# Kernel optimization log

Hardware: AMD Instinct MI355X
Metric: run time of the kernel (lower is better)

Reference implementation:

```python
import jax, jax.numpy as jnp
import numpy as np

B, T, V, H = 512, 200, 99, 256


def setup_inputs() -> dict:
    key = jax.random.key(0)
    ks = jax.random.split(key, 32)
    u01 = lambda k, shp, s: jax.random.uniform(k, shp, jnp.float32, -s, s)
    sV = 1.0 / np.sqrt(V); sH = 1.0 / np.sqrt(H); s2V = 1.0 / np.sqrt(2 * V)
    inp = {
        'x': jax.random.normal(ks[0], (B, T, V), jnp.float32),
        'x_hat': jax.random.normal(ks[1], (B, T, V), jnp.float32),
        'u': jax.random.uniform(ks[2], (B, T, V), jnp.float32),
        'm': (jax.random.uniform(ks[3], (B, T, V)) < 0.8).astype(jnp.float32),  # observation mask
        'd': jax.random.uniform(ks[4], (B, T, V), jnp.float32) * 5.0,  # time deltas >= 0
        'y': jax.random.uniform(ks[5], (B, 1), jnp.float32),
        'W_td': u01(ks[6], (H, V), sV), 'b_td': u01(ks[7], (H,), sV),
        'W_hist': u01(ks[8], (V, H), sH), 'b_hist': u01(ks[9], (V,), sH),
        'W_v': u01(ks[10], (V, V), sV), 'b_v': u01(ks[11], (V,), sV),
        'W_r': u01(ks[12], (V, V), sV), 'b_r': u01(ks[13], (V,), sV),
        'W_u': u01(ks[14], (V, V), sV), 'b_u': u01(ks[15], (V,), sV),
        'conv_w': u01(ks[16], (2,), 1.0 / np.sqrt(2.0)), 'conv_b': u01(ks[17], (1,), 1.0 / np.sqrt(2.0)),
        'W_ih': u01(ks[18], (3 * H, 2 * V), s2V), 'b_ih': u01(ks[19], (3 * H,), s2V),
        'W_hh': u01(ks[20], (3 * H, H), sH), 'b_hh': u01(ks[21], (3 * H,), sH),
        'W_fc': u01(ks[22], (1, H), sH), 'b_fc': u01(ks[23], (1,), sH),
    }
    return inp


def _rin_forward(x, x_hat, u, m, d,
                 W_td, b_td, W_hist, b_hist, W_v, b_v, W_r, b_r, W_u, b_u,
                 conv_w, conv_b, W_ih, b_ih, W_hh, b_hh, W_fc, b_fc):
    mfr = 1.0 - jnp.eye(V, dtype=x.dtype)
    Wv_m = (W_v * mfr).T
    Wr_m = (W_r * mfr).T
    h0 = jnp.zeros((x.shape[0], H), x.dtype)

    def step(carry, inp_t):
        h, loss = carry
        x_t, xh_t, u_t, m_t, d_t = inp_t
        gamma_h = jnp.exp(-jax.nn.relu(d_t @ W_td.T + b_td))  # [B,H]
        h = h * gamma_h
        x_h = h @ W_hist.T + b_hist                            # [B,V]
        x_r_t = m_t * x_t + (1.0 - m_t) * x_h
        xbar = m_t * x_t + (1.0 - m_t) * xh_t
        unc = jnp.exp(-jax.nn.relu(u_t @ W_u.T + b_u))         # unc_flag == 1
        xu = (xbar @ Wv_m + b_v) * unc
        xr = x_r_t @ Wr_m + b_r
        x_comb = conv_w[0] * xu + conv_w[1] * xr + conv_b[0]   # 1x1 conv over channel dim 2
        loss = loss + jnp.sum(jnp.abs(x_t - x_comb) * m_t) / (jnp.sum(m_t) + 1e-5)
        x_imp_t = m_t * x_t + (1.0 - m_t) * x_comb
        gru_in = jnp.concatenate([x_imp_t, m_t], axis=1)       # [B,2V]
        gi = gru_in @ W_ih.T + b_ih                            # [B,3H]
        gh = h @ W_hh.T + b_hh
        r = jax.nn.sigmoid(gi[:, :H] + gh[:, :H])
        z = jax.nn.sigmoid(gi[:, H:2 * H] + gh[:, H:2 * H])
        n = jnp.tanh(gi[:, 2 * H:] + r * gh[:, 2 * H:])
        h = (1.0 - z) * n + z * h
        return (h, loss), (x_imp_t, xu, xr)

    seq = (jnp.swapaxes(x, 0, 1), jnp.swapaxes(x_hat, 0, 1), jnp.swapaxes(u, 0, 1),
           jnp.swapaxes(m, 0, 1), jnp.swapaxes(d, 0, 1))  # [T,B,V] each
    (h, x_loss), (x_imp, xus, xrs) = jax.lax.scan(step, (h0, jnp.float32(0.0)), seq)
    x_imp = jnp.swapaxes(x_imp, 0, 1)  # [B,T,V]
    xus = jnp.swapaxes(xus, 0, 1)
    xrs = jnp.swapaxes(xrs, 0, 1)
    y_out = h @ W_fc.T + b_fc          # task == 'C'
    y_score = jax.nn.sigmoid(y_out)
    return x_imp, y_out, y_score, x_loss, xus, xrs


def reference(x, x_hat, u, m, d, y,
              W_td, b_td, W_hist, b_hist, W_v, b_v, W_r, b_r, W_u, b_u,
              conv_w, conv_b, W_ih, b_ih, W_hh, b_hh, W_fc, b_fc):
    return _rin_forward(x, x_hat, u, m, d,
                        W_td, b_td, W_hist, b_hist, W_v, b_v, W_r, b_r, W_u, b_u,
                        conv_w, conv_b, W_ih, b_ih, W_hh, b_hh, W_fc, b_fc)
```

## Files before the change

### kernel.cpp

```cpp
#include <hip/hip_runtime.h>

typedef unsigned short u16;
typedef unsigned int   u32;
typedef unsigned char  u8;
typedef unsigned long long u64;
typedef long i64;
typedef __attribute__((ext_vector_type(8))) short s16x8;
typedef __attribute__((ext_vector_type(4))) float f32x4;
typedef __attribute__((ext_vector_type(2))) float f32x2;
typedef __attribute__((ext_vector_type(4), aligned(4))) float f32x4u;

#define DEV static __device__ __forceinline__

constexpr int B_ = 512, T_ = 200, V_ = 99, H_ = 256;
constexpr int TV_ = T_ * V_;
constexpr u32 BH_ = B_ * H_;

constexpr long long XIMP_O = 0;
constexpr long long YOUT_O = 10137600;
constexpr long long YSC_O  = 10138112;
constexpr long long LOSS_O = 10138624;
constexpr long long XUS_O  = 10138625;
constexpr long long XRS_O  = 20276225;

constexpr long long WS_MSUM   = 0;
constexpr long long WS_GAMMA  = 1024;
constexpr long long WS_XRPRE  = 52429824;
constexpr long long WS_X16    = 72705024;
constexpr long long WS_XUS16  = 93185024;
constexpr long long WS_M8     = 113460224;
constexpr long long WS_GIM8   = 124109824;
constexpr long long WS_WTD    = 202753024;
constexpr long long WS_WU     = WS_WTD + 65536;
constexpr long long WS_WV     = WS_WU + 28672;
constexpr long long WS_WRB    = WS_WV + 28672;
constexpr long long WS_WIHM_B = WS_WRB + 28672;
constexpr long long WS_F8     = WS_WIHM_B + 196608;
constexpr long long WS_WIHX8  = WS_F8;
constexpr long long WS_WHH8   = WS_F8 + 98304;
constexpr long long WS_WHIST8 = WS_F8 + 294912;
constexpr long long WS_WR8    = WS_F8 + 323584;
constexpr long long WS_LOSSP  = WS_F8 + 337920;

DEV u16 cvt_bf16(float f) {
  union { float f; u32 u; } v; v.f = f;
  u32 u = v.u;
  return (u16)((u + 0x7fffu + ((u >> 16) & 1u)) >> 16);
}
DEV float cvt_f32(u16 h) {
  union { u32 u; float f; } v; v.u = ((u32)h) << 16;
  return v.f;
}
DEV u32 enc_e4m3(float f) {
  union { float f; u32 u; } v; v.f = f;
  u32 sign = (v.u >> 24) & 0x80u;
  v.u &= 0x7fffffffu;
  float a = fminf(v.f, 448.f);
  if (a < 0.015625f) {
    int mq = (int)rintf(a * 512.f);
    return sign | (u32)mq;
  }
  union { float f; u32 u; } w; w.f = a;
  u32 lsb = (w.u >> 20) & 1u;
  u32 r = w.u + 0x7FFFFu + lsb;
  u32 E = ((r >> 23) & 0xffu) - 120u;
  u32 M = (r >> 20) & 7u;
  if (E >= 16u) { E = 15u; M = 6u; }
  return sign | (E << 3) | M;
}
DEV u32 cvtfp8(float a) {
  u32 r;
  asm("v_cvt_pk_fp8_f32 %0, %1, %2" : "=v"(r) : "v"(a), "v"(a));
  return r;
}
DEV u32 cvtfp8x2(float a, float b) {
  u32 r;
  asm("v_cvt_pk_fp8_f32 %0, %1, %2" : "=v"(r) : "v"(a), "v"(b));
  return r & 0xffffu;
}
DEV u32 pkbf(float a, float b) {
  u32 r;
  asm("v_cvt_pk_bf16_f32 %0, %1, %2" : "=v"(r) : "v"(a), "v"(b));
  return r;
}
#if __has_builtin(__builtin_amdgcn_cvt_pk_f32_fp8)
DEV f32x4 dec8x4(u32 w) {
  f32x2 lo = __builtin_amdgcn_cvt_pk_f32_fp8((int)w, false);
  f32x2 hi = __builtin_amdgcn_cvt_pk_f32_fp8((int)w, true);
  return (f32x4){lo[0], lo[1], hi[0], hi[1]};
}
#else
DEV float dec8(u32 b) {
  u32 e = (b >> 3) & 0xfu, mm = b & 7u, s = b >> 7;
  union { u32 u; float f; } v;
  v.u = (s << 31) | ((e + 120u) << 23) | (mm << 20);
  return e ? v.f : 0.f;
}
DEV f32x4 dec8x4(u32 w) {
  return (f32x4){dec8(w & 0xff), dec8((w >> 8) & 0xff), dec8((w >> 16) & 0xff), dec8(w >> 24)};
}
#endif
DEV s16x8 mk8(f32x4 lo, f32x4 hi) {
  union { u32 q[4]; s16x8 v; } u;
  u.q[0] = pkbf(lo[0], lo[1]); u.q[1] = pkbf(lo[2], lo[3]);
  u.q[2] = pkbf(hi[0], hi[1]); u.q[3] = pkbf(hi[2], hi[3]);
  return u.v;
}
DEV f32x4 l4(const float* p) { return (f32x4)(*(const f32x4u*)p); }
DEV f32x4 mfma16(s16x8 a, s16x8 b, f32x4 c) {
  return __builtin_amdgcn_mfma_f32_16x16x32_bf16(a, b, c, 0, 0, 0);
}
DEV f32x4 mfma8(i64 a, i64 b, f32x4 c) {
  return __builtin_amdgcn_mfma_f32_16x16x32_fp8_fp8(a, b, c, 0, 0, 0);
}
DEV s16x8 ldB(const u16* w, int frag, int lane) {
  return *reinterpret_cast<const s16x8*>(w + ((long long)frag * 64 + lane) * 8);
}
DEV float sigm(float v) { return 1.f / (1.f + __expf(-v)); }
DEV float tanhx(float v) {
  float e = __expf(-2.f * fabsf(v));
  float t = (1.f - e) / (1.f + e);
  return v < 0.f ? -t : t;
}

__global__ __launch_bounds__(256) void k0_pack(
    const float* __restrict__ W_td, const float* __restrict__ W_u, const float* __restrict__ W_v,
    const float* __restrict__ W_r, const float* __restrict__ W_ih,
    float* __restrict__ msum, u16* __restrict__ wsu) {
  if (blockIdx.x == 85) {
    if (threadIdx.x < T_) msum[threadIdx.x] = 0.f;
    return;
  }
  int frag = blockIdx.x * 4 + (threadIdx.x >> 6);
  int lane = threadIdx.x & 63;
  const float* src; long long off; int koff, kmax, nmax, stride, diag = 0, f;
  if (frag < 64)       { f = frag;       src = W_td; off = WS_WTD;    stride = 99;  koff = 0;  kmax = 99; nmax = 256; }
  else if (frag < 92)  { f = frag - 64;  src = W_u;  off = WS_WU;     stride = 99;  koff = 0;  kmax = 99; nmax = 99;  }
  else if (frag < 120) { f = frag - 92;  src = W_v;  off = WS_WV;     stride = 99;  koff = 0;  kmax = 99; nmax = 99;  diag = 1; }
  else if (frag < 148) { f = frag - 120; src = W_r;  off = WS_WRB;    stride = 99;  koff = 0;  kmax = 99; nmax = 99;  diag = 1; }
  else if (frag < 340) { f = frag - 148; src = W_ih; off = WS_WIHM_B; stride = 198; koff = 99; kmax = 99; nmax = 768; }
  else return;
  int nt = f / 4, kc = f % 4;
  int n = nt * 16 + (lane & 15);
  u16* dst = wsu + off / 2 + ((long long)f * 64 + lane) * 8;
#pragma unroll
  for (int j = 0; j < 8; j++) {
    int k = kc * 32 + ((lane >> 4) << 3) + j;
    float v = 0.f;
    if (k < kmax && n < nmax && !(diag && k == n)) v = src[(long long)n * stride + koff + k];
    dst[j] = cvt_bf16(v);
  }
}

__global__ __launch_bounds__(256) void k0b_pack8(
    const float* __restrict__ W_ih, const float* __restrict__ W_hh,
    const float* __restrict__ W_hist, const float* __restrict__ W_r, u8* __restrict__ ws8) {
  int frag = blockIdx.x * 4 + (threadIdx.x >> 6);
  int lane = threadIdx.x & 63;
  const float* src; long long off; int KC, kmax, nmax, stride, diag = 0, f;
  if (frag < 192)      { f = frag;       src = W_ih;   off = WS_WIHX8;  KC = 4; stride = 198; kmax = 99;  nmax = 768; }
  else if (frag < 576) { f = frag - 192; src = W_hh;   off = WS_WHH8;   KC = 8; stride = 256; kmax = 256; nmax = 768; }
  else if (frag < 632) { f = frag - 576; src = W_hist; off = WS_WHIST8; KC = 8; stride = 256; kmax = 256; nmax = 99;  }
  else if (frag < 660) { f = frag - 632; src = W_r;    off = WS_WR8;    KC = 4; stride = 99;  kmax = 99;  nmax = 99;  diag = 1; }
  else return;
  int nt = f / KC, kc = f % KC;
  int n = nt * 16 + (lane & 15);
  u64 r = 0;
#pragma unroll
  for (int j = 0; j < 8; j++) {
    int k = kc * 32 + ((lane >> 4) << 3) + j;
    float v = 0.f;
    if (k < kmax && n < nmax && !(diag && k == n)) v = src[(long long)n * stride + k] * 16.f;
    r |= (u64)enc_e4m3(v) << (8 * j);
  }
  *reinterpret_cast<u64*>(ws8 + off + ((long long)f * 64 + lane) * 8) = r;
}

__global__ __launch_bounds__(256) void k2_pre(
    const float* __restrict__ x, const float* __restrict__ xh, const float* __restrict__ uu,
    const float* __restrict__ m, const float* __restrict__ dd,
    const float* __restrict__ b_td, const float* __restrict__ b_u, const float* __restrict__ b_v,
    const float* __restrict__ b_r, const float* __restrict__ b_ih,
    float* __restrict__ msum, float* __restrict__ out, u16* __restrict__ wsu) {
  const int tid = threadIdx.x, w = tid >> 6, lane = tid & 63;
  const int bc = blockIdx.x & 31, tg = blockIdx.x >> 5;
  const int t = tg * 4 + w;
  const int b0 = bc * 16;
  const int cl = lane & 15, rq = (lane >> 4) << 2, kr8 = (lane >> 4) << 3;
  const long long gb = (long long)(b0 + cl) * TV_ + (long long)t * V_;
  u8* ws8 = reinterpret_cast<u8*>(wsu);
  const u16* wtd   = wsu + WS_WTD / 2;
  const u16* wu    = wsu + WS_WU / 2;
  const u16* wv    = wsu + WS_WV / 2;
  const u16* wrb   = wsu + WS_WRB / 2;
  const u16* wihmb = wsu + WS_WIHM_B / 2;
  u16* gam = wsu + WS_GAMMA / 2;
  u16* xrp = wsu + WS_XRPRE / 2;
  u16* x16p = wsu + WS_X16 / 2;
  u16* xu16p = wsu + WS_XUS16 / 2;
  u8* m8p = ws8 + WS_M8;
  u8* gim8p = ws8 + WS_GIM8;
  const f32x4 z4 = {0.f, 0.f, 0.f, 0.f};

  {
    s16x8 fd[4];
#pragma unroll
    for (int kc = 0; kc < 3; kc++) {
      int k0 = kc * 32 + kr8;
      fd[kc] = mk8(l4(dd + gb + k0), l4(dd + gb + k0 + 4));
    }
    {
      f32x4 a = z4;
      if (kr8 == 0) { a[0] = dd[gb + 96]; a[1] = dd[gb + 97]; a[2] = dd[gb + 98]; }
      fd[3] = mk8(a, z4);
    }
    for (int nt = 0; nt < 16; nt++) {
      int col = nt * 16 + cl;
      float bt = b_td[col];
      f32x4 a = {bt, bt, bt, bt};
#pragma unroll
      for (int kc = 0; kc < 4; kc++) a = mfma16(fd[kc], ldB(wtd, nt * 4 + kc, lane), a);
#pragma unroll
      for (int j = 0; j < 4; j++) {
        int b = b0 + rq + j;
        gam[((long long)t * B_ + b) * H_ + col] = cvt_bf16(__expf(-fmaxf(a[j], 0.f)));
      }
    }
  }

  s16x8 fu[4], fxb[4], fmx[4], fm[4];
  float mpart = 0.f;
  const long long rowoff = (long long)t * B_ + (b0 + cl);
  u16* x16row = x16p + rowoff * 100;
  u8* m8row = m8p + rowoff * 104;
#pragma unroll
  for (int kc = 0; kc < 3; kc++) {
    int k0 = kc * 32 + kr8;
    f32x4 u0 = l4(uu + gb + k0), u1 = l4(uu + gb + k0 + 4);
    f32x4 m0 = l4(m + gb + k0),  m1 = l4(m + gb + k0 + 4);
    f32x4 x0 = l4(x + gb + k0),  x1 = l4(x + gb + k0 + 4);
    f32x4 h0 = l4(xh + gb + k0), h1 = l4(xh + gb + k0 + 4);
    fu[kc]  = mk8(u0, u1);
    fm[kc]  = mk8(m0, m1);
    fmx[kc] = mk8(m0 * x0, m1 * x1);
    fxb[kc] = mk8(h0 + m0 * (x0 - h0), h1 + m1 * (x1 - h1));
    mpart += m0[0] + m0[1] + m0[2] + m0[3] + m1[0] + m1[1] + m1[2] + m1[3];
    u64 xw0 = (u64)pkbf(x0[0], x0[1]) | ((u64)pkbf(x0[2], x0[3]) << 32);
    u64 xw1 = (u64)pkbf(x1[0], x1[1]) | ((u64)pkbf(x1[2], x1[3]) << 32);
    *reinterpret_cast<u64*>(x16row + k0) = xw0;
    *reinterpret_cast<u64*>(x16row + k0 + 4) = xw1;
    u64 mb = 0;
#pragma unroll
    for (int e = 0; e < 4; e++) {
      mb |= (m0[e] > 0.5f ? 0x50ull : 0ull) << (8 * e);
      mb |= (m1[e] > 0.5f ? 0x50ull : 0ull) << (32 + 8 * e);
    }
    *reinterpret_cast<u64*>(m8row + k0) = mb;
  }
  {
    f32x4 u0 = z4, m0 = z4, x0 = z4, h0 = z4;
    if (kr8 == 0) {
#pragma unroll
      for (int e = 0; e < 3; e++) {
        u0[e] = uu[gb + 96 + e]; m0[e] = m[gb + 96 + e];
        x0[e] = x[gb + 96 + e];  h0[e] = xh[gb + 96 + e];
      }
#pragma unroll
      for (int e = 0; e < 3; e++) {
        x16row[96 + e] = cvt_bf16(x0[e]);
        m8row[96 + e] = (m0[e] > 0.5f) ? 0x50 : 0;
      }
    }
    fu[3]  = mk8(u0, z4);
    fm[3]  = mk8(m0, z4);
    fmx[3] = mk8(m0 * x0, z4);
    fxb[3] = mk8(h0 + m0 * (x0 - h0), z4);
    mpart += m0[0] + m0[1] + m0[2];
  }
  {
    float mp = mpart;
#pragma unroll
    for (int s = 32; s; s >>= 1) mp += __shfl_xor(mp, s);
    if (lane == 0) atomicAdd(&msum[t], mp);
  }

  for (int nt = 0; nt < 7; nt++) {
    int col = nt * 16 + cl;
    float bu_ = 0.f, bv_ = 0.f, br_ = 0.f;
    if (col < V_) { bu_ = b_u[col]; bv_ = b_v[col]; br_ = b_r[col]; }
    f32x4 au = {bu_, bu_, bu_, bu_}, av = {bv_, bv_, bv_, bv_}, ar = {br_, br_, br_, br_};
#pragma unroll
    for (int kc = 0; kc < 4; kc++) {
      au = mfma16(fu[kc],  ldB(wu, nt * 4 + kc, lane), au);
      av = mfma16(fxb[kc], ldB(wv, nt * 4 + kc, lane), av);
      ar = mfma16(fmx[kc], ldB(wrb, nt * 4 + kc, lane), ar);
    }
    if (col < V_) {
#pragma unroll
      for (int j = 0; j < 4; j++) {
        int b = b0 + rq + j;
        float unc = __expf(-fmaxf(au[j], 0.f));
        float xuv = av[j] * unc;
        out[XUS_O + (long long)b * TV_ + (long long)t * V_ + col] = xuv;
        xu16p[((long long)t * B_ + b) * V_ + col] = cvt_bf16(xuv);
        xrp[((long long)t * B_ + b) * V_ + col] = cvt_bf16(ar[j]);
      }
    }
  }
  for (int nt = 0; nt < 48; nt++) {
    int col = nt * 16 + cl;
    float bi = b_ih[col];
    f32x4 a = {bi, bi, bi, bi};
#pragma unroll
    for (int kc = 0; kc < 4; kc++) a = mfma16(fm[kc], ldB(wihmb, nt * 4 + kc, lane), a);
    u32 p = cvtfp8x2(a[0] * 64.f, a[1] * 64.f) | (cvtfp8x2(a[2] * 64.f, a[3] * 64.f) << 16);
    *reinterpret_cast<u32*>(gim8p + (((long long)t * 32 + bc) * 48 + nt) * 256 + (long long)lane * 4) = p;
  }
}

__global__ void __attribute__((amdgpu_flat_work_group_size(1024, 1024), amdgpu_waves_per_eu(4, 4)))
k_seq(
    const float* __restrict__ b_hist, const float* __restrict__ b_hh,
    const float* __restrict__ conv_w, const float* __restrict__ conv_b,
    const float* __restrict__ W_fc, const float* __restrict__ b_fc,
    const float* __restrict__ msum, float* out, u16* wsu) {
  __shared__ __align__(16) u8 hp8_s[16 * 272];
  __shared__ __align__(16) u8 e8_s[16 * 144];
  __shared__ __align__(16) u8 xi8_s[16 * 144];
  __shared__ __align__(16) u8 whhR_l[65536];
  __shared__ __align__(16) u8 whist8_l[28672];
  __shared__ __align__(16) u8 wr8_l[14336];
  __shared__ __align__(16) float hf_s[8][260];
  __shared__ float red_s[1024];

  const int tid = threadIdx.x, wv = tid >> 6, lane = tid & 63;
  const int cl = lane & 15, rq = (lane >> 4) << 2, kr8 = (lane >> 4) << 3;
  const int b0 = blockIdx.x * 8;
  const int cc = blockIdx.x >> 1, half = blockIdx.x & 1;
  const u8* ws8 = reinterpret_cast<const u8*>(wsu);

  for (int i = tid; i < 1088; i += 1024) reinterpret_cast<u32*>(hp8_s)[i] = 0;
  for (int i = tid; i < 576; i += 1024) { reinterpret_cast<u32*>(e8_s)[i] = 0; reinterpret_cast<u32*>(xi8_s)[i] = 0; }
  {
    const u32* s0 = reinterpret_cast<const u32*>(ws8 + WS_WHH8);
    u32* d0 = reinterpret_cast<u32*>(whhR_l);
    for (int i = tid; i < 16384; i += 1024) d0[i] = s0[i];
    const u32* s1 = reinterpret_cast<const u32*>(ws8 + WS_WHIST8);
    u32* d1 = reinterpret_cast<u32*>(whist8_l);
    for (int i = tid; i < 7168; i += 1024) d1[i] = s1[i];
    const u32* s2 = reinterpret_cast<const u32*>(ws8 + WS_WR8);
    u32* d2 = reinterpret_cast<u32*>(wr8_l);
    for (int i = tid; i < 3584; i += 1024) d2[i] = s2[i];
  }

  const u64* wx8 = reinterpret_cast<const u64*>(ws8 + WS_WIHX8);
  const u64* wh8 = reinterpret_cast<const u64*>(ws8 + WS_WHH8);
  i64 wihx_r[3][4];
  i64 whhZ[8], whhN[8];
#pragma unroll
  for (int gg = 0; gg < 3; gg++)
#pragma unroll
    for (int kc = 0; kc < 4; kc++)
      wihx_r[gg][kc] = (i64)wx8[(long long)((gg * 16 + wv) * 4 + kc) * 64 + lane];
#pragma unroll
  for (int kc = 0; kc < 8; kc++) {
    whhZ[kc] = (i64)wh8[(long long)((16 + wv) * 8 + kc) * 64 + lane];
    whhN[kc] = (i64)wh8[(long long)((32 + wv) * 8 + kc) * 64 + lane];
  }

  const int col = wv * 16 + cl;
  const float bhh0 = b_hh[col], bhh1 = b_hh[256 + col], bhh2 = b_hh[512 + col];
  const bool vwave = (wv < 7);
  const int vcol = col;
  const bool rowok = (rq < 8);
  const bool vact = vwave && (vcol < V_);
  const bool vld = vact && rowok;
  const float bh = vact ? b_hist[vcol] : 0.f;
  const float cw0 = conv_w[0], cw1 = conv_w[1], cb = conv_b[0];

  const u16* gamp = wsu + WS_GAMMA / 2;
  const u16* x16p = wsu + WS_X16 / 2;
  const u16* xu16p = wsu + WS_XUS16 / 2;
  const u16* xrpp = wsu + WS_XRPRE / 2;
  const u8* m8p = ws8 + WS_M8;
  int lane_p = ((half * 2 + (rq >> 2)) * 16 + cl) & 63;
  const u8* gimp = ws8 + WS_GIM8 + (((long long)cc * 48 + wv) * 64 + lane_p) * 4;

  u32 gaidx = BH_ + (u32)(b0 + rq) * H_ + col;
  u32 xidx = (u32)(b0 + rq) * 100 + vcol;
  u32 xuidx = (u32)(b0 + rq) * 99 + vcol;
  u32 midx = (u32)(b0 + rq) * 104 + vcol;
  u32 gidx = (u32)(b0 + rq) * TV_ + vcol;

  float hpr[4] = {0.f, 0.f, 0.f, 0.f};
  float loss_acc = 0.f;
  constexpr float inv128 = 1.f / 128.f;
  constexpr float inv64 = 1.f / 64.f;
  const f32x4 z4 = {0.f, 0.f, 0.f, 0.f};
  const float* xup_dummy = nullptr; (void)xup_dummy;
  __syncthreads();

  for (int t = 0; t < T_; t++) {
    u32 gimw0, gimw1, gimw2;
    {
      const u32* gp = reinterpret_cast<const u32*>(gimp + (long long)t * 393216);
      gimw0 = gp[0]; gimw1 = gp[1024]; gimw2 = gp[2048];
    }
    u16 ga[4] = {0, 0, 0, 0};
    if (rowok) {
#pragma unroll
      for (int j = 0; j < 4; j++) ga[j] = gamp[gaidx + (u32)j * H_];
    }
    gaidx += BH_;
    u16 cx16[4] = {0, 0, 0, 0}, cxu[4] = {0, 0, 0, 0}, cxr[4] = {0, 0, 0, 0};
    u8 cm8[4] = {0, 0, 0, 0};
    if (vld) {
#pragma unroll
      for (int j = 0; j < 4; j++) {
        cx16[j] = x16p[xidx + (u32)j * 100];
        cxu[j]  = xu16p[xuidx + (u32)j * 99];
        cxr[j]  = xrpp[xuidx + (u32)j * 99];
        cm8[j]  = m8p[midx + (u32)j * 104];
      }
    }
    xidx += B_ * 100; xuidx += B_ * 99; midx += B_ * 104;
    const float msv = msum[t];

    f32x4 accR = z4, accZ = z4, accNh = z4, accXh = z4;
#pragma unroll
    for (int kc = 0; kc < 8; kc++) {
      const i64 a = *reinterpret_cast<const i64*>(&hp8_s[cl * 272 + kc * 32 + kr8]);
      const i64 br = *reinterpret_cast<const i64*>(&whhR_l[(wv * 8 + kc) * 512 + lane * 8]);
      accR  = mfma8(a, br, accR);
      accZ  = mfma8(a, whhZ[kc], accZ);
      accNh = mfma8(a, whhN[kc], accNh);
      if (vwave) {
        const i64 bw = *reinterpret_cast<const i64*>(&whist8_l[(wv * 8 + kc) * 512 + lane * 8]);
        accXh = mfma8(a, bw, accXh);
      }
    }
    if (vld) {
#pragma unroll
      for (int j = 0; j < 4; j++) {
        const float xhv = accXh[j] * inv128 + bh;
        const float ev = cm8[j] ? 0.f : xhv;
        e8_s[(rq + j) * 144 + vcol] = (u8)cvtfp8(ev * 8.f);
      }
    }
    __syncthreads();

    if (vwave) {
      f32x4 acc = z4;
#pragma unroll
      for (int kc = 0; kc < 4; kc++) {
        const i64 a = *reinterpret_cast<const i64*>(&e8_s[cl * 144 + kc * 32 + kr8]);
        const i64 b = *reinterpret_cast<const i64*>(&wr8_l[(wv * 4 + kc) * 512 + lane * 8]);
        acc = mfma8(a, b, acc);
      }
      if (vld) {
        const float inv_ms = 1.f / (msv + 1e-5f);
        float ls = 0.f;
#pragma unroll
        for (int j = 0; j < 4; j++) {
          const float xrv = acc[j] * inv128 + cvt_f32(cxr[j]);
          const float xc = cw0 * cvt_f32(cxu[j]) + cw1 * xrv + cb;
          const float xj = cvt_f32(cx16[j]);
          const bool mj = cm8[j] != 0;
          const float ximp = mj ? xj : xc;
          ls += mj ? fabsf(xj - xc) : 0.f;
          const u32 gj = gidx + (u32)j * TV_;
          out[XIMP_O + gj] = ximp;
          out[XRS_O + gj] = xrv;
          xi8_s[(rq + j) * 144 + vcol] = (u8)cvtfp8(ximp * 8.f);
        }
        loss_acc += ls * inv_ms;
      }
    }
    gidx += V_;
    __syncthreads();

    f32x4 accNx = z4;
#pragma unroll
    for (int kc = 0; kc < 4; kc++) {
      const i64 a = *reinterpret_cast<const i64*>(&xi8_s[cl * 144 + kc * 32 + kr8]);
      accR  = mfma8(a, wihx_r[0][kc], accR);
      accZ  = mfma8(a, wihx_r[1][kc], accZ);
      accNx = mfma8(a, wihx_r[2][kc], accNx);
    }
    const f32x4 gimR = dec8x4(gimw0);
    const f32x4 gimZ = dec8x4(gimw1);
    const f32x4 gimN = dec8x4(gimw2);
#pragma unroll
    for (int j = 0; j < 4; j++) {
      const float rr = sigm(accR[j] * inv128 + gimR[j] * inv64 + bhh0);
      const float zz = sigm(accZ[j] * inv128 + gimZ[j] * inv64 + bhh1);
      const float gin = accNx[j] * inv128 + gimN[j] * inv64;
      const float ghn = accNh[j] * inv128 + bhh2;
      const float nn = tanhx(gin + rr * ghn);
      const float hn = (1.f - zz) * nn + zz * hpr[j];
      if (t + 1 < T_) {
        const float hpnew = hn * cvt_f32(ga[j]);
        hpr[j] = hpnew;
        if (rowok) hp8_s[(rq + j) * 272 + col] = (u8)cvtfp8(hpnew * 8.f);
      } else {
        if (rowok) hf_s[rq + j][col] = hn;
      }
    }
    __syncthreads();
  }

  if (tid < 8) {
    float acc = 0.f;
    for (int k = 0; k < H_; k++) acc += hf_s[tid][k] * W_fc[k];
    const float yv = acc + b_fc[0];
    out[YOUT_O + b0 + tid] = yv;
    out[YSC_O + b0 + tid] = 1.f / (1.f + __expf(-yv));
  }
  red_s[tid] = loss_acc;
  __syncthreads();
  for (int s = 512; s; s >>= 1) {
    if (tid < s) red_s[tid] += red_s[tid + s];
    __syncthreads();
  }
  if (tid == 0) {
    float* lp = reinterpret_cast<float*>(reinterpret_cast<char*>(wsu) + WS_LOSSP);
    lp[blockIdx.x] = red_s[0];
  }
}

__global__ void k3_loss(const float* __restrict__ lossp, float* __restrict__ out) {
  if (threadIdx.x == 0) {
    float s = 0.f;
    for (int i = 0; i < 64; i++) s += lossp[i];
    out[LOSS_O] = s;
  }
}

extern "C" void kernel_launch(void* const* d_in, const int* in_sizes, int n_in,
                              void* d_out, int out_size, void* d_ws, size_t ws_size,
                              hipStream_t stream) {
  (void)in_sizes; (void)n_in; (void)out_size; (void)ws_size;
  const float* x      = (const float*)d_in[0];
  const float* xhat   = (const float*)d_in[1];
  const float* u      = (const float*)d_in[2];
  const float* m      = (const float*)d_in[3];
  const float* d      = (const float*)d_in[4];
  const float* W_td   = (const float*)d_in[6];
  const float* b_td   = (const float*)d_in[7];
  const float* W_hist = (const float*)d_in[8];
  const float* b_hist = (const float*)d_in[9];
  const float* W_v    = (const float*)d_in[10];
  const float* b_v    = (const float*)d_in[11];
  const float* W_r    = (const float*)d_in[12];
  const float* b_r    = (const float*)d_in[13];
  const float* W_u    = (const float*)d_in[14];
  const float* b_u    = (const float*)d_in[15];
  const float* conv_w = (const float*)d_in[16];
  const float* conv_b = (const float*)d_in[17];
  const float* W_ih   = (const float*)d_in[18];
  const float* b_ih   = (const float*)d_in[19];
  const float* W_hh   = (const float*)d_in[20];
  const float* b_hh   = (const float*)d_in[21];
  const float* W_fc   = (const float*)d_in[22];
  const float* b_fc   = (const float*)d_in[23];
  float* out = (float*)d_out;
  u16* wsu = (u16*)d_ws;
  float* msum = (float*)d_ws;
  const float* lossp = (const float*)((char*)d_ws + WS_LOSSP);

  hipLaunchKernelGGL(k0_pack, dim3(86), dim3(256), 0, stream,
                     W_td, W_u, W_v, W_r, W_ih, msum, wsu);
  hipLaunchKernelGGL(k0b_pack8, dim3(165), dim3(256), 0, stream,
                     W_ih, W_hh, W_hist, W_r, (u8*)d_ws);
  hipLaunchKernelGGL(k2_pre, dim3(1600), dim3(256), 0, stream,
                     x, xhat, u, m, d, b_td, b_u, b_v, b_r, b_ih, msum, out, wsu);
  hipLaunchKernelGGL(k_seq, dim3(64), dim3(1024), 0, stream,
                     b_hist, b_hh, conv_w, conv_b, W_fc, b_fc, msum, out, wsu);
  hipLaunchKernelGGL(k3_loss, dim3(1), dim3(64), 0, stream, lossp, out);
}
```

Baseline: 1.321 ms.

## Prefetch next-step inputs, move x_hist MFMA to idle waves, use LDS-only barriers

Loads the gate and imputation inputs (gim, x, xu, xr, mask) for step t+1 during step t and rotates them through registers, so global-load latency leaves the serial recurrence's critical path. The x_hist MFMA and the e8 write move from waves 0-6 to waves 9-15, which also carry the V-stage work less, to balance per-wave load. __syncthreads is replaced by a barrier that waits only on LDS counters, so pending global stores and loads no longer stall it. This adds register pressure and relies on the custom barrier being a correct fence for the shared-memory traffic.

```diff
diff --git a/kernel.cpp b/kernel.cpp
--- a/kernel.cpp
+++ b/kernel.cpp
@@ -121,6 +121,9 @@
   float e = __expf(-2.f * fabsf(v));
   float t = (1.f - e) / (1.f + e);
   return v < 0.f ? -t : t;
+}
+DEV void barL() {
+  asm volatile("s_waitcnt lgkmcnt(0)\n\ts_barrier" ::: "memory");
 }
 
 __global__ __launch_bounds__(256) void k0_pack(
@@ -370,12 +373,17 @@
 
   const int col = wv * 16 + cl;
   const float bhh0 = b_hh[col], bhh1 = b_hh[256 + col], bhh2 = b_hh[512 + col];
+  const bool rowok = (rq < 8);
   const bool vwave = (wv < 7);
   const int vcol = col;
-  const bool rowok = (rq < 8);
   const bool vact = vwave && (vcol < V_);
   const bool vld = vact && rowok;
-  const float bh = vact ? b_hist[vcol] : 0.f;
+  const int xw = wv - 9;
+  const bool ewave = (wv >= 9);
+  const int ecol = xw * 16 + cl;
+  const bool eact = ewave && (ecol < V_);
+  const bool eld = eact && rowok;
+  const float bhE = eact ? b_hist[ecol] : 0.f;
   const float cw0 = conv_w[0], cw1 = conv_w[1], cb = conv_b[0];
 
   const u16* gamp = wsu + WS_GAMMA / 2;
@@ -384,46 +392,73 @@
   const u16* xrpp = wsu + WS_XRPRE / 2;
   const u8* m8p = ws8 + WS_M8;
   int lane_p = ((half * 2 + (rq >> 2)) * 16 + cl) & 63;
-  const u8* gimp = ws8 + WS_GIM8 + (((long long)cc * 48 + wv) * 64 + lane_p) * 4;
+  const u32* gimp = reinterpret_cast<const u32*>(ws8 + WS_GIM8 + (((long long)cc * 48 + wv) * 64 + lane_p) * 4);
 
   u32 gaidx = BH_ + (u32)(b0 + rq) * H_ + col;
   u32 xidx = (u32)(b0 + rq) * 100 + vcol;
   u32 xuidx = (u32)(b0 + rq) * 99 + vcol;
   u32 midx = (u32)(b0 + rq) * 104 + vcol;
+  u32 emidx = (u32)(b0 + rq) * 104 + ecol;
   u32 gidx = (u32)(b0 + rq) * TV_ + vcol;
+  constexpr u32 GIMSTEP = 98304;
 
   float hpr[4] = {0.f, 0.f, 0.f, 0.f};
   float loss_acc = 0.f;
   constexpr float inv128 = 1.f / 128.f;
   constexpr float inv64 = 1.f / 64.f;
   const f32x4 z4 = {0.f, 0.f, 0.f, 0.f};
-  const float* xup_dummy = nullptr; (void)xup_dummy;
+
+  u32 gimC0 = 0, gimC1 = 0, gimC2 = 0;
+  u16 cxC[4] = {0, 0, 0, 0}, cxuC[4] = {0, 0, 0, 0}, cxrC[4] = {0, 0, 0, 0};
+  u8 cmC[4] = {0, 0, 0, 0}, emC[4] = {0, 0, 0, 0};
+  {
+    gimC0 = gimp[0]; gimC1 = gimp[1024]; gimC2 = gimp[2048];
+    if (vld) {
+#pragma unroll
+      for (int j = 0; j < 4; j++) {
+        cxC[j]  = x16p[xidx + (u32)j * 100];
+        cxuC[j] = xu16p[xuidx + (u32)j * 99];
+        cxrC[j] = xrpp[xuidx + (u32)j * 99];
+        cmC[j]  = m8p[midx + (u32)j * 104];
+      }
+    }
+    if (eld) {
+#pragma unroll
+      for (int j = 0; j < 4; j++) emC[j] = m8p[emidx + (u32)j * 104];
+    }
+  }
   __syncthreads();
 
   for (int t = 0; t < T_; t++) {
-    u32 gimw0, gimw1, gimw2;
-    {
-      const u32* gp = reinterpret_cast<const u32*>(gimp + (long long)t * 393216);
-      gimw0 = gp[0]; gimw1 = gp[1024]; gimw2 = gp[2048];
-    }
+    u32 gimN0 = 0, gimN1 = 0, gimN2 = 0;
+    u16 cxN[4] = {0, 0, 0, 0}, cxuN[4] = {0, 0, 0, 0}, cxrN[4] = {0, 0, 0, 0};
+    u8 cmN[4] = {0, 0, 0, 0}, emN[4] = {0, 0, 0, 0};
+    if (t + 1 < T_) {
+      const u32* gp = gimp + (u32)(t + 1) * GIMSTEP;
+      gimN0 = gp[0]; gimN1 = gp[1024]; gimN2 = gp[2048];
+      const u32 xi2 = xidx + B_ * 100, xui2 = xuidx + B_ * 99;
+      const u32 mi2 = midx + B_ * 104, emi2 = emidx + B_ * 104;
+      if (vld) {
+#pragma unroll
+        for (int j = 0; j < 4; j++) {
+          cxN[j]  = x16p[xi2 + (u32)j * 100];
+          cxuN[j] = xu16p[xui2 + (u32)j * 99];
+          cxrN[j] = xrpp[xui2 + (u32)j * 99];
+          cmN[j]  = m8p[mi2 + (u32)j * 104];
+        }
+      }
+      if (eld) {
+#pragma unroll
+        for (int j = 0; j < 4; j++) emN[j] = m8p[emi2 + (u32)j * 104];
+      }
+    }
+    xidx += B_ * 100; xuidx += B_ * 99; midx += B_ * 104; emidx += B_ * 104;
     u16 ga[4] = {0, 0, 0, 0};
-    if (rowok) {
+    if (rowok && t + 1 < T_) {
 #pragma unroll
       for (int j = 0; j < 4; j++) ga[j] = gamp[gaidx + (u32)j * H_];
     }
     gaidx += BH_;
-    u16 cx16[4] = {0, 0, 0, 0}, cxu[4] = {0, 0, 0, 0}, cxr[4] = {0, 0, 0, 0};
-    u8 cm8[4] = {0, 0, 0, 0};
-    if (vld) {
-#pragma unroll
-      for (int j = 0; j < 4; j++) {
-        cx16[j] = x16p[xidx + (u32)j * 100];
-        cxu[j]  = xu16p[xuidx + (u32)j * 99];
-        cxr[j]  = xrpp[xuidx + (u32)j * 99];
-        cm8[j]  = m8p[midx + (u32)j * 104];
-      }
-    }
-    xidx += B_ * 100; xuidx += B_ * 99; midx += B_ * 104;
     const float msv = msum[t];
 
     f32x4 accR = z4, accZ = z4, accNh = z4, accXh = z4;
@@ -434,20 +469,20 @@
       accR  = mfma8(a, br, accR);
       accZ  = mfma8(a, whhZ[kc], accZ);
       accNh = mfma8(a, whhN[kc], accNh);
-      if (vwave) {
-        const i64 bw = *reinterpret_cast<const i64*>(&whist8_l[(wv * 8 + kc) * 512 + lane * 8]);
+      if (ewave) {
+        const i64 bw = *reinterpret_cast<const i64*>(&whist8_l[(xw * 8 + kc) * 512 + lane * 8]);
         accXh = mfma8(a, bw, accXh);
       }
     }
-    if (vld) {
+    if (eld) {
 #pragma unroll
       for (int j = 0; j < 4; j++) {
-        const float xhv = accXh[j] * inv128 + bh;
-        const float ev = cm8[j] ? 0.f : xhv;
-        e8_s[(rq + j) * 144 + vcol] = (u8)cvtfp8(ev * 8.f);
-      }
-    }
-    __syncthreads();
+        const float xhv = accXh[j] * inv128 + bhE;
+        const float ev = emC[j] ? 0.f : xhv;
+        e8_s[(rq + j) * 144 + ecol] = (u8)cvtfp8(ev * 8.f);
+      }
+    }
+    barL();
 
     if (vwave) {
       f32x4 acc = z4;
@@ -462,10 +497,10 @@
         float ls = 0.f;
 #pragma unroll
         for (int j = 0; j < 4; j++) {
-          const float xrv = acc[j] * inv128 + cvt_f32(cxr[j]);
-          const float xc = cw0 * cvt_f32(cxu[j]) + cw1 * xrv + cb;
-          const float xj = cvt_f32(cx16[j]);
-          const bool mj = cm8[j] != 0;
+          const float xrv = acc[j] * inv128 + cvt_f32(cxrC[j]);
+          const float xc = cw0 * cvt_f32(cxuC[j]) + cw1 * xrv + cb;
+          const float xj = cvt_f32(cxC[j]);
+          const bool mj = cmC[j] != 0;
           const float ximp = mj ? xj : xc;
           ls += mj ? fabsf(xj - xc) : 0.f;
           const u32 gj = gidx + (u32)j * TV_;
@@ -477,7 +512,7 @@
       }
     }
     gidx += V_;
-    __syncthreads();
+    barL();
 
     f32x4 accNx = z4;
 #pragma unroll
@@ -487,9 +522,9 @@
       accZ  = mfma8(a, wihx_r[1][kc], accZ);
       accNx = mfma8(a, wihx_r[2][kc], accNx);
     }
-    const f32x4 gimR = dec8x4(gimw0);
-    const f32x4 gimZ = dec8x4(gimw1);
-    const f32x4 gimN = dec8x4(gimw2);
+    const f32x4 gimR = dec8x4(gimC0);
+    const f32x4 gimZ = dec8x4(gimC1);
+    const f32x4 gimN = dec8x4(gimC2);
 #pragma unroll
     for (int j = 0; j < 4; j++) {
       const float rr = sigm(accR[j] * inv128 + gimR[j] * inv64 + bhh0);
@@ -506,7 +541,13 @@
         if (rowok) hf_s[rq + j][col] = hn;
       }
     }
-    __syncthreads();
+    gimC0 = gimN0; gimC1 = gimN1; gimC2 = gimN2;
+#pragma unroll
+    for (int j = 0; j < 4; j++) {
+      cxC[j] = cxN[j]; cxuC[j] = cxuN[j]; cxrC[j] = cxrN[j];
+      cmC[j] = cmN[j]; emC[j] = emN[j];
+    }
+    barL();
   }
 
   if (tid < 8) {
```

New measurement: 1.659 ms. 1.26x slower.

## Add per-timestep ready counters so sequential kernel overlaps precompute kernel

Applied to the files above, without the earlier changes.

The precompute kernel now increments a per-timestep counter (agent-scope release atomic) as each block finishes its timestep. The sequential GRU kernel spin-waits on the counter for the next timestep, so it can start before all precompute work is done. Global stores of x_imp and xrs are moved after the barrier so they overlap the following MFMA work. The benefit depends on both kernels running at the same time; with serialized launches it only adds atomic and polling overhead, and co-residency assumptions risk a deadlock.

```diff
diff --git a/kernel.cpp b/kernel.cpp
--- a/kernel.cpp
+++ b/kernel.cpp
@@ -41,6 +41,7 @@
 constexpr long long WS_WHIST8 = WS_F8 + 294912;
 constexpr long long WS_WR8    = WS_F8 + 323584;
 constexpr long long WS_LOSSP  = WS_F8 + 337920;
+constexpr long long WS_TCNT   = WS_F8 + 338176;
 
 DEV u16 cvt_bf16(float f) {
   union { float f; u32 u; } v; v.f = f;
@@ -128,7 +129,8 @@
     const float* __restrict__ W_r, const float* __restrict__ W_ih,
     float* __restrict__ msum, u16* __restrict__ wsu) {
   if (blockIdx.x == 85) {
-    if (threadIdx.x < T_) msum[threadIdx.x] = 0.f;
+    u32* tcount = reinterpret_cast<u32*>(reinterpret_cast<u8*>(wsu) + WS_TCNT);
+    if (threadIdx.x < T_) { msum[threadIdx.x] = 0.f; tcount[threadIdx.x] = 0; }
     return;
   }
   int frag = blockIdx.x * 4 + (threadIdx.x >> 6);
@@ -200,6 +202,7 @@
   u16* xu16p = wsu + WS_XUS16 / 2;
   u8* m8p = ws8 + WS_M8;
   u8* gim8p = ws8 + WS_GIM8;
+  u32* tcount = reinterpret_cast<u32*>(ws8 + WS_TCNT);
   const f32x4 z4 = {0.f, 0.f, 0.f, 0.f};
 
   {
@@ -316,6 +319,9 @@
     u32 p = cvtfp8x2(a[0] * 64.f, a[1] * 64.f) | (cvtfp8x2(a[2] * 64.f, a[3] * 64.f) << 16);
     *reinterpret_cast<u32*>(gim8p + (((long long)t * 32 + bc) * 48 + nt) * 256 + (long long)lane * 4) = p;
   }
+  if (lane == 0) {
+    __hip_atomic_fetch_add(&tcount[t], 1u, __ATOMIC_RELEASE, __HIP_MEMORY_SCOPE_AGENT);
+  }
 }
 
 __global__ void __attribute__((amdgpu_flat_work_group_size(1024, 1024), amdgpu_waves_per_eu(4, 4)))
@@ -338,6 +344,7 @@
   const int b0 = blockIdx.x * 8;
   const int cc = blockIdx.x >> 1, half = blockIdx.x & 1;
   const u8* ws8 = reinterpret_cast<const u8*>(wsu);
+  const u32* tcount = reinterpret_cast<const u32*>(ws8 + WS_TCNT);
 
   for (int i = tid; i < 1088; i += 1024) reinterpret_cast<u32*>(hp8_s)[i] = 0;
   for (int i = tid; i < 576; i += 1024) { reinterpret_cast<u32*>(e8_s)[i] = 0; reinterpret_cast<u32*>(xi8_s)[i] = 0; }
@@ -370,9 +377,9 @@
 
   const int col = wv * 16 + cl;
   const float bhh0 = b_hh[col], bhh1 = b_hh[256 + col], bhh2 = b_hh[512 + col];
+  const bool rowok = (rq < 8);
   const bool vwave = (wv < 7);
   const int vcol = col;
-  const bool rowok = (rq < 8);
   const bool vact = vwave && (vcol < V_);
   const bool vld = vact && rowok;
   const float bh = vact ? b_hist[vcol] : 0.f;
@@ -397,17 +404,25 @@
   constexpr float inv128 = 1.f / 128.f;
   constexpr float inv64 = 1.f / 64.f;
   const f32x4 z4 = {0.f, 0.f, 0.f, 0.f};
-  const float* xup_dummy = nullptr; (void)xup_dummy;
+
+  while (__hip_atomic_load(&tcount[0], __ATOMIC_ACQUIRE, __HIP_MEMORY_SCOPE_AGENT) != 32u) {
+    __builtin_amdgcn_s_sleep(8);
+  }
   __syncthreads();
 
   for (int t = 0; t < T_; t++) {
+    if (t + 1 < T_) {
+      while (__hip_atomic_load(&tcount[t + 1], __ATOMIC_ACQUIRE, __HIP_MEMORY_SCOPE_AGENT) != 32u) {
+        __builtin_amdgcn_s_sleep(8);
+      }
+    }
     u32 gimw0, gimw1, gimw2;
     {
       const u32* gp = reinterpret_cast<const u32*>(gimp + (long long)t * 393216);
       gimw0 = gp[0]; gimw1 = gp[1024]; gimw2 = gp[2048];
     }
     u16 ga[4] = {0, 0, 0, 0};
-    if (rowok) {
+    if (rowok && t + 1 < T_) {
 #pragma unroll
       for (int j = 0; j < 4; j++) ga[j] = gamp[gaidx + (u32)j * H_];
     }
@@ -449,6 +464,7 @@
     }
     __syncthreads();
 
+    float ximp_h[4], xrv_h[4];
     if (vwave) {
       f32x4 acc = z4;
 #pragma unroll
@@ -468,17 +484,24 @@
           const bool mj = cm8[j] != 0;
           const float ximp = mj ? xj : xc;
           ls += mj ? fabsf(xj - xc) : 0.f;
-          const u32 gj = gidx + (u32)j * TV_;
-          out[XIMP_O + gj] = ximp;
-          out[XRS_O + gj] = xrv;
+          ximp_h[j] = ximp;
+          xrv_h[j] = xrv;
           xi8_s[(rq + j) * 144 + vcol] = (u8)cvtfp8(ximp * 8.f);
         }
         loss_acc += ls * inv_ms;
       }
     }
+    __syncthreads();
+
+    if (vld) {
+#pragma unroll
+      for (int j = 0; j < 4; j++) {
+        const u32 gj = gidx + (u32)j * TV_;
+        out[XIMP_O + gj] = ximp_h[j];
+        out[XRS_O + gj] = xrv_h[j];
+      }
+    }
     gidx += V_;
-    __syncthreads();
-
     f32x4 accNx = z4;
 #pragma unroll
     for (int kc = 0; kc < 4; kc++) {
```

New measurement: 2.017 ms. 52.7% more time.

## Fuse mask-half of GRU input projection into sequential kernel via FP8 MFMA

Applied to the files above, without the earlier changes.

The mask-dependent part of the GRU input projection (m_t @ W_ih[:,V:] + b_ih) was computed in the parallel pre-pass and stored as an FP8 tensor that the sequential kernel read back at every step. It is now computed inside the sequential loop. The mask is staged in shared memory and multiplied by FP8-packed W_ih mask weights held in registers, adding three extra MFMAs per K-chunk. This removes a large workspace write and a per-step global read, at the cost of more register pressure and compute on the serial critical path. The b_ih and b_hh biases are pre-summed, and the gamma load is skipped on the last step.

```diff
diff --git a/kernel.cpp b/kernel.cpp
--- a/kernel.cpp
+++ b/kernel.cpp
@@ -29,18 +29,17 @@
 constexpr long long WS_X16    = 72705024;
 constexpr long long WS_XUS16  = 93185024;
 constexpr long long WS_M8     = 113460224;
-constexpr long long WS_GIM8   = 124109824;
 constexpr long long WS_WTD    = 202753024;
 constexpr long long WS_WU     = WS_WTD + 65536;
 constexpr long long WS_WV     = WS_WU + 28672;
 constexpr long long WS_WRB    = WS_WV + 28672;
-constexpr long long WS_WIHM_B = WS_WRB + 28672;
-constexpr long long WS_F8     = WS_WIHM_B + 196608;
+constexpr long long WS_F8     = WS_WRB + 28672;
 constexpr long long WS_WIHX8  = WS_F8;
 constexpr long long WS_WHH8   = WS_F8 + 98304;
 constexpr long long WS_WHIST8 = WS_F8 + 294912;
 constexpr long long WS_WR8    = WS_F8 + 323584;
-constexpr long long WS_LOSSP  = WS_F8 + 337920;
+constexpr long long WS_WIHM8  = WS_F8 + 337920;
+constexpr long long WS_LOSSP  = WS_F8 + 436224;
 
 DEV u16 cvt_bf16(float f) {
   union { float f; u32 u; } v; v.f = f;
@@ -73,33 +72,11 @@
   asm("v_cvt_pk_fp8_f32 %0, %1, %2" : "=v"(r) : "v"(a), "v"(a));
   return r;
 }
-DEV u32 cvtfp8x2(float a, float b) {
-  u32 r;
-  asm("v_cvt_pk_fp8_f32 %0, %1, %2" : "=v"(r) : "v"(a), "v"(b));
-  return r & 0xffffu;
-}
 DEV u32 pkbf(float a, float b) {
   u32 r;
   asm("v_cvt_pk_bf16_f32 %0, %1, %2" : "=v"(r) : "v"(a), "v"(b));
   return r;
 }
-#if __has_builtin(__builtin_amdgcn_cvt_pk_f32_fp8)
-DEV f32x4 dec8x4(u32 w) {
-  f32x2 lo = __builtin_amdgcn_cvt_pk_f32_fp8((int)w, false);
-  f32x2 hi = __builtin_amdgcn_cvt_pk_f32_fp8((int)w, true);
-  return (f32x4){lo[0], lo[1], hi[0], hi[1]};
-}
-#else
-DEV float dec8(u32 b) {
-  u32 e = (b >> 3) & 0xfu, mm = b & 7u, s = b >> 7;
-  union { u32 u; float f; } v;
-  v.u = (s << 31) | ((e + 120u) << 23) | (mm << 20);
-  return e ? v.f : 0.f;
-}
-DEV f32x4 dec8x4(u32 w) {
-  return (f32x4){dec8(w & 0xff), dec8((w >> 8) & 0xff), dec8((w >> 16) & 0xff), dec8(w >> 24)};
-}
-#endif
 DEV s16x8 mk8(f32x4 lo, f32x4 hi) {
   union { u32 q[4]; s16x8 v; } u;
   u.q[0] = pkbf(lo[0], lo[1]); u.q[1] = pkbf(lo[2], lo[3]);
@@ -125,20 +102,19 @@
 
 __global__ __launch_bounds__(256) void k0_pack(
     const float* __restrict__ W_td, const float* __restrict__ W_u, const float* __restrict__ W_v,
-    const float* __restrict__ W_r, const float* __restrict__ W_ih,
+    const float* __restrict__ W_r,
     float* __restrict__ msum, u16* __restrict__ wsu) {
-  if (blockIdx.x == 85) {
+  if (blockIdx.x == 37) {
     if (threadIdx.x < T_) msum[threadIdx.x] = 0.f;
     return;
   }
   int frag = blockIdx.x * 4 + (threadIdx.x >> 6);
   int lane = threadIdx.x & 63;
-  const float* src; long long off; int koff, kmax, nmax, stride, diag = 0, f;
-  if (frag < 64)       { f = frag;       src = W_td; off = WS_WTD;    stride = 99;  koff = 0;  kmax = 99; nmax = 256; }
-  else if (frag < 92)  { f = frag - 64;  src = W_u;  off = WS_WU;     stride = 99;  koff = 0;  kmax = 99; nmax = 99;  }
-  else if (frag < 120) { f = frag - 92;  src = W_v;  off = WS_WV;     stride = 99;  koff = 0;  kmax = 99; nmax = 99;  diag = 1; }
-  else if (frag < 148) { f = frag - 120; src = W_r;  off = WS_WRB;    stride = 99;  koff = 0;  kmax = 99; nmax = 99;  diag = 1; }
-  else if (frag < 340) { f = frag - 148; src = W_ih; off = WS_WIHM_B; stride = 198; koff = 99; kmax = 99; nmax = 768; }
+  const float* src; long long off; int kmax, nmax, stride, diag = 0, f;
+  if (frag < 64)       { f = frag;       src = W_td; off = WS_WTD; stride = 99; kmax = 99; nmax = 256; }
+  else if (frag < 92)  { f = frag - 64;  src = W_u;  off = WS_WU;  stride = 99; kmax = 99; nmax = 99;  }
+  else if (frag < 120) { f = frag - 92;  src = W_v;  off = WS_WV;  stride = 99; kmax = 99; nmax = 99;  diag = 1; }
+  else if (frag < 148) { f = frag - 120; src = W_r;  off = WS_WRB; stride = 99; kmax = 99; nmax = 99;  diag = 1; }
   else return;
   int nt = f / 4, kc = f % 4;
   int n = nt * 16 + (lane & 15);
@@ -147,7 +123,7 @@
   for (int j = 0; j < 8; j++) {
     int k = kc * 32 + ((lane >> 4) << 3) + j;
     float v = 0.f;
-    if (k < kmax && n < nmax && !(diag && k == n)) v = src[(long long)n * stride + koff + k];
+    if (k < kmax && n < nmax && !(diag && k == n)) v = src[(long long)n * stride + k];
     dst[j] = cvt_bf16(v);
   }
 }
@@ -157,11 +133,12 @@
     const float* __restrict__ W_hist, const float* __restrict__ W_r, u8* __restrict__ ws8) {
   int frag = blockIdx.x * 4 + (threadIdx.x >> 6);
   int lane = threadIdx.x & 63;
-  const float* src; long long off; int KC, kmax, nmax, stride, diag = 0, f;
-  if (frag < 192)      { f = frag;       src = W_ih;   off = WS_WIHX8;  KC = 4; stride = 198; kmax = 99;  nmax = 768; }
-  else if (frag < 576) { f = frag - 192; src = W_hh;   off = WS_WHH8;   KC = 8; stride = 256; kmax = 256; nmax = 768; }
-  else if (frag < 632) { f = frag - 576; src = W_hist; off = WS_WHIST8; KC = 8; stride = 256; kmax = 256; nmax = 99;  }
-  else if (frag < 660) { f = frag - 632; src = W_r;    off = WS_WR8;    KC = 4; stride = 99;  kmax = 99;  nmax = 99;  diag = 1; }
+  const float* src; long long off; int KC, koff, kmax, nmax, stride, diag = 0, f;
+  if (frag < 192)      { f = frag;       src = W_ih;   off = WS_WIHX8;  KC = 4; stride = 198; koff = 0; kmax = 99;  nmax = 768; }
+  else if (frag < 576) { f = frag - 192; src = W_hh;   off = WS_WHH8;   KC = 8; stride = 256; koff = 0; kmax = 256; nmax = 768; }
+  else if (frag < 632) { f = frag - 576; src = W_hist; off = WS_WHIST8; KC = 8; stride = 256; koff = 0; kmax = 256; nmax = 99;  }
+  else if (frag < 660) { f = frag - 632; src = W_r;    off = WS_WR8;    KC = 4; stride = 99;  koff = 0; kmax = 99;  nmax = 99;  diag = 1; }
+  else if (frag < 852) { f = frag - 660; src = W_ih;   off = WS_WIHM8;  KC = 4; stride = 198; koff = 99; kmax = 99; nmax = 768; }
   else return;
   int nt = f / KC, kc = f % KC;
   int n = nt * 16 + (lane & 15);
@@ -170,7 +147,7 @@
   for (int j = 0; j < 8; j++) {
     int k = kc * 32 + ((lane >> 4) << 3) + j;
     float v = 0.f;
-    if (k < kmax && n < nmax && !(diag && k == n)) v = src[(long long)n * stride + k] * 16.f;
+    if (k < kmax && n < nmax && !(diag && k == n)) v = src[(long long)n * stride + koff + k] * 16.f;
     r |= (u64)enc_e4m3(v) << (8 * j);
   }
   *reinterpret_cast<u64*>(ws8 + off + ((long long)f * 64 + lane) * 8) = r;
@@ -180,7 +157,7 @@
     const float* __restrict__ x, const float* __restrict__ xh, const float* __restrict__ uu,
     const float* __restrict__ m, const float* __restrict__ dd,
     const float* __restrict__ b_td, const float* __restrict__ b_u, const float* __restrict__ b_v,
-    const float* __restrict__ b_r, const float* __restrict__ b_ih,
+    const float* __restrict__ b_r,
     float* __restrict__ msum, float* __restrict__ out, u16* __restrict__ wsu) {
   const int tid = threadIdx.x, w = tid >> 6, lane = tid & 63;
   const int bc = blockIdx.x & 31, tg = blockIdx.x >> 5;
@@ -189,17 +166,15 @@
   const int cl = lane & 15, rq = (lane >> 4) << 2, kr8 = (lane >> 4) << 3;
   const long long gb = (long long)(b0 + cl) * TV_ + (long long)t * V_;
   u8* ws8 = reinterpret_cast<u8*>(wsu);
-  const u16* wtd   = wsu + WS_WTD / 2;
-  const u16* wu    = wsu + WS_WU / 2;
-  const u16* wv    = wsu + WS_WV / 2;
-  const u16* wrb   = wsu + WS_WRB / 2;
-  const u16* wihmb = wsu + WS_WIHM_B / 2;
+  const u16* wtd = wsu + WS_WTD / 2;
+  const u16* wu  = wsu + WS_WU / 2;
+  const u16* wv  = wsu + WS_WV / 2;
+  const u16* wrb = wsu + WS_WRB / 2;
   u16* gam = wsu + WS_GAMMA / 2;
   u16* xrp = wsu + WS_XRPRE / 2;
   u16* x16p = wsu + WS_X16 / 2;
   u16* xu16p = wsu + WS_XUS16 / 2;
   u8* m8p = ws8 + WS_M8;
-  u8* gim8p = ws8 + WS_GIM8;
   const f32x4 z4 = {0.f, 0.f, 0.f, 0.f};
 
   {
@@ -228,7 +203,7 @@
     }
   }
 
-  s16x8 fu[4], fxb[4], fmx[4], fm[4];
+  s16x8 fu[4], fxb[4], fmx[4];
   float mpart = 0.f;
   const long long rowoff = (long long)t * B_ + (b0 + cl);
   u16* x16row = x16p + rowoff * 100;
@@ -241,7 +216,6 @@
     f32x4 x0 = l4(x + gb + k0),  x1 = l4(x + gb + k0 + 4);
     f32x4 h0 = l4(xh + gb + k0), h1 = l4(xh + gb + k0 + 4);
     fu[kc]  = mk8(u0, u1);
-    fm[kc]  = mk8(m0, m1);
     fmx[kc] = mk8(m0 * x0, m1 * x1);
     fxb[kc] = mk8(h0 + m0 * (x0 - h0), h1 + m1 * (x1 - h1));
     mpart += m0[0] + m0[1] + m0[2] + m0[3] + m1[0] + m1[1] + m1[2] + m1[3];
@@ -272,7 +246,6 @@
       }
     }
     fu[3]  = mk8(u0, z4);
-    fm[3]  = mk8(m0, z4);
     fmx[3] = mk8(m0 * x0, z4);
     fxb[3] = mk8(h0 + m0 * (x0 - h0), z4);
     mpart += m0[0] + m0[1] + m0[2];
@@ -307,26 +280,18 @@
       }
     }
   }
-  for (int nt = 0; nt < 48; nt++) {
-    int col = nt * 16 + cl;
-    float bi = b_ih[col];
-    f32x4 a = {bi, bi, bi, bi};
-#pragma unroll
-    for (int kc = 0; kc < 4; kc++) a = mfma16(fm[kc], ldB(wihmb, nt * 4 + kc, lane), a);
-    u32 p = cvtfp8x2(a[0] * 64.f, a[1] * 64.f) | (cvtfp8x2(a[2] * 64.f, a[3] * 64.f) << 16);
-    *reinterpret_cast<u32*>(gim8p + (((long long)t * 32 + bc) * 48 + nt) * 256 + (long long)lane * 4) = p;
-  }
 }
 
 __global__ void __attribute__((amdgpu_flat_work_group_size(1024, 1024), amdgpu_waves_per_eu(4, 4)))
 k_seq(
-    const float* __restrict__ b_hist, const float* __restrict__ b_hh,
+    const float* __restrict__ b_hist, const float* __restrict__ b_ih, const float* __restrict__ b_hh,
     const float* __restrict__ conv_w, const float* __restrict__ conv_b,
     const float* __restrict__ W_fc, const float* __restrict__ b_fc,
     const float* __restrict__ msum, float* out, u16* wsu) {
   __shared__ __align__(16) u8 hp8_s[16 * 272];
   __shared__ __align__(16) u8 e8_s[16 * 144];
   __shared__ __align__(16) u8 xi8_s[16 * 144];
+  __shared__ __align__(16) u8 m8_s[16 * 144];
   __shared__ __align__(16) u8 whhR_l[65536];
   __shared__ __align__(16) u8 whist8_l[28672];
   __shared__ __align__(16) u8 wr8_l[14336];
@@ -336,11 +301,14 @@
   const int tid = threadIdx.x, wv = tid >> 6, lane = tid & 63;
   const int cl = lane & 15, rq = (lane >> 4) << 2, kr8 = (lane >> 4) << 3;
   const int b0 = blockIdx.x * 8;
-  const int cc = blockIdx.x >> 1, half = blockIdx.x & 1;
   const u8* ws8 = reinterpret_cast<const u8*>(wsu);
 
   for (int i = tid; i < 1088; i += 1024) reinterpret_cast<u32*>(hp8_s)[i] = 0;
-  for (int i = tid; i < 576; i += 1024) { reinterpret_cast<u32*>(e8_s)[i] = 0; reinterpret_cast<u32*>(xi8_s)[i] = 0; }
+  for (int i = tid; i < 576; i += 1024) {
+    reinterpret_cast<u32*>(e8_s)[i] = 0;
+    reinterpret_cast<u32*>(xi8_s)[i] = 0;
+    reinterpret_cast<u32*>(m8_s)[i] = 0;
+  }
   {
     const u32* s0 = reinterpret_cast<const u32*>(ws8 + WS_WHH8);
     u32* d0 = reinterpret_cast<u32*>(whhR_l);
@@ -354,14 +322,17 @@
   }
 
   const u64* wx8 = reinterpret_cast<const u64*>(ws8 + WS_WIHX8);
+  const u64* wm8 = reinterpret_cast<const u64*>(ws8 + WS_WIHM8);
   const u64* wh8 = reinterpret_cast<const u64*>(ws8 + WS_WHH8);
-  i64 wihx_r[3][4];
+  i64 wihx_r[3][4], wihm_r[3][4];
   i64 whhZ[8], whhN[8];
 #pragma unroll
   for (int gg = 0; gg < 3; gg++)
 #pragma unroll
-    for (int kc = 0; kc < 4; kc++)
+    for (int kc = 0; kc < 4; kc++) {
       wihx_r[gg][kc] = (i64)wx8[(long long)((gg * 16 + wv) * 4 + kc) * 64 + lane];
+      wihm_r[gg][kc] = (i64)wm8[(long long)((gg * 16 + wv) * 4 + kc) * 64 + lane];
+    }
 #pragma unroll
   for (int kc = 0; kc < 8; kc++) {
     whhZ[kc] = (i64)wh8[(long long)((16 + wv) * 8 + kc) * 64 + lane];
@@ -369,10 +340,13 @@
   }
 
   const int col = wv * 16 + cl;
-  const float bhh0 = b_hh[col], bhh1 = b_hh[256 + col], bhh2 = b_hh[512 + col];
+  const float bs0 = b_ih[col] + b_hh[col];
+  const float bs1 = b_ih[256 + col] + b_hh[256 + col];
+  const float bin = b_ih[512 + col];
+  const float bhn = b_hh[512 + col];
+  const bool rowok = (rq < 8);
   const bool vwave = (wv < 7);
   const int vcol = col;
-  const bool rowok = (rq < 8);
   const bool vact = vwave && (vcol < V_);
   const bool vld = vact && rowok;
   const float bh = vact ? b_hist[vcol] : 0.f;
@@ -383,8 +357,6 @@
   const u16* xu16p = wsu + WS_XUS16 / 2;
   const u16* xrpp = wsu + WS_XRPRE / 2;
   const u8* m8p = ws8 + WS_M8;
-  int lane_p = ((half * 2 + (rq >> 2)) * 16 + cl) & 63;
-  const u8* gimp = ws8 + WS_GIM8 + (((long long)cc * 48 + wv) * 64 + lane_p) * 4;
 
   u32 gaidx = BH_ + (u32)(b0 + rq) * H_ + col;
   u32 xidx = (u32)(b0 + rq) * 100 + vcol;
@@ -395,19 +367,12 @@
   float hpr[4] = {0.f, 0.f, 0.f, 0.f};
   float loss_acc = 0.f;
   constexpr float inv128 = 1.f / 128.f;
-  constexpr float inv64 = 1.f / 64.f;
   const f32x4 z4 = {0.f, 0.f, 0.f, 0.f};
-  const float* xup_dummy = nullptr; (void)xup_dummy;
   __syncthreads();
 
   for (int t = 0; t < T_; t++) {
-    u32 gimw0, gimw1, gimw2;
-    {
-      const u32* gp = reinterpret_cast<const u32*>(gimp + (long long)t * 393216);
-      gimw0 = gp[0]; gimw1 = gp[1024]; gimw2 = gp[2048];
-    }
     u16 ga[4] = {0, 0, 0, 0};
-    if (rowok) {
+    if (rowok && t + 1 < T_) {
 #pragma unroll
       for (int j = 0; j < 4; j++) ga[j] = gamp[gaidx + (u32)j * H_];
     }
@@ -472,6 +437,7 @@
           out[XIMP_O + gj] = ximp;
           out[XRS_O + gj] = xrv;
           xi8_s[(rq + j) * 144 + vcol] = (u8)cvtfp8(ximp * 8.f);
+          m8_s[(rq + j) * 144 + vcol] = cm8[j];
         }
         loss_acc += ls * inv_ms;
       }
@@ -486,16 +452,17 @@
       accR  = mfma8(a, wihx_r[0][kc], accR);
       accZ  = mfma8(a, wihx_r[1][kc], accZ);
       accNx = mfma8(a, wihx_r[2][kc], accNx);
-    }
-    const f32x4 gimR = dec8x4(gimw0);
-    const f32x4 gimZ = dec8x4(gimw1);
-    const f32x4 gimN = dec8x4(gimw2);
+      const i64 am = *reinterpret_cast<const i64*>(&m8_s[cl * 144 + kc * 32 + kr8]);
+      accR  = mfma8(am, wihm_r[0][kc], accR);
+      accZ  = mfma8(am, wihm_r[1][kc], accZ);
+      accNx = mfma8(am, wihm_r[2][kc], accNx);
+    }
 #pragma unroll
     for (int j = 0; j < 4; j++) {
-      const float rr = sigm(accR[j] * inv128 + gimR[j] * inv64 + bhh0);
-      const float zz = sigm(accZ[j] * inv128 + gimZ[j] * inv64 + bhh1);
-      const float gin = accNx[j] * inv128 + gimN[j] * inv64;
-      const float ghn = accNh[j] * inv128 + bhh2;
+      const float rr = sigm(accR[j] * inv128 + bs0);
+      const float zz = sigm(accZ[j] * inv128 + bs1);
+      const float gin = accNx[j] * inv128 + bin;
+      const float ghn = accNh[j] * inv128 + bhn;
       const float nn = tanhx(gin + rr * ghn);
       const float hn = (1.f - zz) * nn + zz * hpr[j];
       if (t + 1 < T_) {
@@ -568,13 +535,13 @@
   float* msum = (float*)d_ws;
   const float* lossp = (const float*)((char*)d_ws + WS_LOSSP);
 
-  hipLaunchKernelGGL(k0_pack, dim3(86), dim3(256), 0, stream,
-                     W_td, W_u, W_v, W_r, W_ih, msum, wsu);
-  hipLaunchKernelGGL(k0b_pack8, dim3(165), dim3(256), 0, stream,
+  hipLaunchKernelGGL(k0_pack, dim3(38), dim3(256), 0, stream,
+                     W_td, W_u, W_v, W_r, msum, wsu);
+  hipLaunchKernelGGL(k0b_pack8, dim3(213), dim3(256), 0, stream,
                      W_ih, W_hh, W_hist, W_r, (u8*)d_ws);
   hipLaunchKernelGGL(k2_pre, dim3(1600), dim3(256), 0, stream,
-                     x, xhat, u, m, d, b_td, b_u, b_v, b_r, b_ih, msum, out, wsu);
+                     x, xhat, u, m, d, b_td, b_u, b_v, b_r, msum, out, wsu);
   hipLaunchKernelGGL(k_seq, dim3(64), dim3(1024), 0, stream,
-                     b_hist, b_hh, conv_w, conv_b, W_fc, b_fc, msum, out, wsu);
+                     b_hist, b_ih, b_hh, conv_w, conv_b, W_fc, b_fc, msum, out, wsu);
   hipLaunchKernelGGL(k3_loss, dim3(1), dim3(64), 0, stream, lossp, out);
 }
```

Measured after the change: 1.373 ms. +3.9%, slower.
